# Optimization experiments

Hardware: AMD Instinct MI355X
Metric: run time of the kernel (lower is better)

The kernel has to match this reference:

```python
import jax, jax.numpy as jnp
import numpy as np

BS = 4
EMBED = 256
HEADS = 8
LEVELS = 4
POINTS = 4
HD = EMBED // HEADS  # 32
SHAPES = np.array([[96, 96], [48, 48], [24, 24], [12, 12]], dtype=np.int64)
LQ = int((SHAPES[:, 0] * SHAPES[:, 1]).sum())  # 12240


def _offset_bias():
    # faithful to MSDeformableAttention._reset_parameters grid init
    thetas = np.arange(HEADS, dtype=np.float32) * (2.0 * np.pi / HEADS)
    g = np.stack([np.cos(thetas), np.sin(thetas)], -1)
    g = g / np.abs(g).max(-1, keepdims=True)
    g = np.tile(g.reshape(HEADS, 1, 1, 2), (1, LEVELS, POINTS, 1))
    g = g * np.arange(1, POINTS + 1, dtype=np.float32).reshape(1, 1, -1, 1)
    return jnp.asarray(g.reshape(-1), dtype=jnp.float32)


def setup_inputs() -> dict:
    key = jax.random.key(0)
    ks = jax.random.split(key, 8)
    tp = HEADS * LEVELS * POINTS
    d = {}
    d["query"] = jax.random.normal(ks[0], (BS, LQ, EMBED), jnp.float32)
    d["reference_points"] = jax.random.uniform(ks[1], (BS, LQ, LEVELS, 2), jnp.float32)
    d["value"] = jax.random.normal(ks[2], (BS, LQ, EMBED), jnp.float32)
    d["value_spatial_shapes"] = SHAPES  # static numpy, int
    d["W_off"] = jax.random.normal(ks[3], (EMBED, tp * 2), jnp.float32) * 0.01
    d["b_off"] = _offset_bias()
    d["W_attn"] = jax.random.normal(ks[4], (EMBED, tp), jnp.float32) * 0.02
    d["b_attn"] = jnp.zeros((tp,), jnp.float32)
    d["W_val"] = jax.random.normal(ks[5], (EMBED, EMBED), jnp.float32) * (1.0 / np.sqrt(EMBED).astype(np.float32))
    d["b_val"] = jnp.zeros((EMBED,), jnp.float32)
    d["W_out"] = jax.random.normal(ks[6], (EMBED, EMBED), jnp.float32) * (1.0 / np.sqrt(EMBED).astype(np.float32))
    d["b_out"] = jnp.zeros((EMBED,), jnp.float32)
    return d


def _bilinear_sample(img, grid):
    # img: [B,H,W,C]; grid: [B,Q,P,2] in [-1,1] (x,y)
    # matches F.grid_sample(mode='bilinear', padding_mode='zeros', align_corners=False)
    B, H, W, C = img.shape
    gx = (grid[..., 0] + 1.0) * (W * 0.5) - 0.5
    gy = (grid[..., 1] + 1.0) * (H * 0.5) - 0.5
    x0 = jnp.floor(gx)
    y0 = jnp.floor(gy)
    wx = gx - x0
    wy = gy - y0
    x0i = x0.astype(jnp.int32)
    y0i = y0.astype(jnp.int32)
    x1i = x0i + 1
    y1i = y0i + 1
    flat = img.reshape(B, H * W, C)

    def corner(xi, yi, w):
        valid = (xi >= 0) & (xi < W) & (yi >= 0) & (yi < H)
        idx = jnp.clip(yi, 0, H - 1) * W + jnp.clip(xi, 0, W - 1)
        v = jnp.take_along_axis(flat, idx.reshape(B, -1, 1), axis=1)
        v = v.reshape(idx.shape + (C,))
        return v * (w * valid)[..., None]

    return (corner(x0i, y0i, (1.0 - wx) * (1.0 - wy))
            + corner(x1i, y0i, wx * (1.0 - wy))
            + corner(x0i, y1i, (1.0 - wx) * wy)
            + corner(x1i, y1i, wx * wy))


def reference(query, reference_points, value, value_spatial_shapes,
              W_off, b_off, W_attn, b_attn, W_val, b_val, W_out, b_out):
    shapes = np.asarray(value_spatial_shapes)  # static [L,2] (H,W)
    bs, Lq, _ = query.shape
    v = (value @ W_val + b_val).reshape(bs, -1, HEADS, HD)  # [bs,Lv,H,hd]
    off = (query @ W_off + b_off).reshape(bs, Lq, HEADS, LEVELS, POINTS, 2)
    aw = jax.nn.softmax((query @ W_attn + b_attn).reshape(bs, Lq, HEADS, LEVELS * POINTS), axis=-1)
    aw = aw.reshape(bs, Lq, HEADS, LEVELS, POINTS)
    # normalizer is (W,H) per level
    norm = jnp.asarray(shapes[:, ::-1].copy(), jnp.float32).reshape(1, 1, 1, LEVELS, 1, 2)
    loc = reference_points[:, :, None, :, None, :] + off / norm
    grids = 2.0 * loc - 1.0  # [bs,Lq,H,L,P,2]

    acc = jnp.zeros((bs * HEADS, Lq, HD), query.dtype)
    start = 0
    for lvl in range(LEVELS):
        h, w = int(shapes[lvl, 0]), int(shapes[lvl, 1])
        v_l = v[:, start:start + h * w].reshape(bs, h, w, HEADS, HD)
        v_l = v_l.transpose(0, 3, 1, 2, 4).reshape(bs * HEADS, h, w, HD)
        g_l = grids[:, :, :, lvl].transpose(0, 2, 1, 3, 4).reshape(bs * HEADS, Lq, POINTS, 2)
        s_l = _bilinear_sample(v_l, g_l)  # [bs*H, Lq, P, hd]
        w_l = aw[:, :, :, lvl].transpose(0, 2, 1, 3).reshape(bs * HEADS, Lq, POINTS)
        acc = acc + jnp.einsum('bqpc,bqp->bqc', s_l, w_l)
        start += h * w

    out = acc.reshape(bs, HEADS, Lq, HD).transpose(0, 2, 1, 3).reshape(bs, Lq, EMBED)
    return out @ W_out + b_out
```

## Files before the change

### kernel.cpp

```cpp
#include <hip/hip_runtime.h>
#include <hip/hip_bf16.h>

static constexpr int BS     = 4;
static constexpr int EMBED  = 256;
static constexpr int HEADS  = 8;
static constexpr int LEVELS = 4;
static constexpr int POINTS = 4;
static constexpr int HD     = 32;
static constexpr int LQ     = 12240;
static constexpr int NROW   = BS * LQ;
static constexpr int LVL_W[4]  = {96, 48, 24, 12};
static constexpr int LVL_H[4]  = {96, 48, 24, 12};
static constexpr int LVL_ST[4] = {0, 9216, 11520, 12096};

typedef __attribute__((ext_vector_type(8))) short short8;
typedef __attribute__((ext_vector_type(4))) float f32x4;
typedef __attribute__((ext_vector_type(2))) float f32x2;

__device__ __forceinline__ unsigned short f2bf(float f) {
    unsigned int u = __float_as_uint(f);
    unsigned int r = (u + 0x7FFFu + ((u >> 16) & 1u)) >> 16;
    return (unsigned short)r;
}

__device__ __forceinline__ void pkfma(f32x2& a, f32x2 v, f32x2 w) {
    asm("v_pk_fma_f32 %0, %1, %2, %0" : "+v"(a) : "v"(v), "v"(w));
}

__global__ __launch_bounds__(256) void prep_weights(
    const float* __restrict__ W_off, const float* __restrict__ W_attn,
    const float* __restrict__ W_val, const float* __restrict__ W_out,
    unsigned short* __restrict__ WT_oa, unsigned short* __restrict__ WT_val,
    unsigned short* __restrict__ WT_out)
{
    const int gid = blockIdx.x * 256 + threadIdx.x;
    const int k = gid & 255;
    const int n = gid >> 8;
    if (n < 384) {
        const float v = (n < 256) ? W_off[k * 256 + n] : W_attn[k * 128 + (n - 256)];
        WT_oa[n * 256 + k] = f2bf(v);
    } else if (n < 640) {
        const int nn = n - 384;
        WT_val[nn * 256 + k] = f2bf(W_val[k * 256 + nn]);
    } else {
        const int nn = n - 640;
        WT_out[nn * 256 + k] = f2bf(W_out[k * 256 + nn]);
    }
}

__global__ __launch_bounds__(256, 5) void gemm_vo(
    const float* __restrict__ Aval, const float* __restrict__ Aqry,
    const unsigned short* __restrict__ Wval, const unsigned short* __restrict__ Woa,
    const float* __restrict__ bval, const float* __restrict__ boff,
    const float* __restrict__ battn,
    unsigned short* __restrict__ Vout, float* __restrict__ OAout)
{
    constexpr int NTW = 2;
    constexpr int NB  = 128;
    constexpr int K   = 256;
    __shared__ __align__(16) unsigned short As[64][40];
    __shared__ __align__(16) unsigned short Bs[NB][40];

    const int x    = blockIdx.x;
    const bool isV = (x < 2);
    const float* A = isV ? Aval : Aqry;
    const unsigned short* Wt = isV ? Wval : Woa;
    const int n0   = isV ? x * 128 : (x - 2) * 128;

    const int tid = threadIdx.x;
    const int m0 = blockIdx.y * 64;
    const int w  = tid >> 6;
    const int l  = tid & 63;
    const int lm = l & 15;
    const int lq = l >> 4;

    const int sr = tid >> 2;
    const int kg = (tid & 3) * 8;

    float4 pa0, pa1;
    short8 pb[NTW];

    auto gload = [&](int k0) {
        const float* ap = &A[(size_t)(m0 + sr) * K + k0 + kg];
        pa0 = *(const float4*)ap;
        pa1 = *(const float4*)(ap + 4);
        #pragma unroll
        for (int i = 0; i < NTW; ++i) {
            const int slot = tid + i * 256;
            const int n  = slot >> 2;
            const int kk = (slot & 3) * 8;
            pb[i] = *(const short8*)&Wt[(size_t)(n0 + n) * K + k0 + kk];
        }
    };

    f32x4 acc[4][NTW];
    #pragma unroll
    for (int rg = 0; rg < 4; ++rg)
        #pragma unroll
        for (int nt = 0; nt < NTW; ++nt)
            acc[rg][nt] = (f32x4){0.f, 0.f, 0.f, 0.f};

    gload(0);
    #pragma unroll 2
    for (int k0 = 0; k0 < K; k0 += 32) {
        uint4 pk;
        pk.x = (unsigned int)f2bf(pa0.x) | ((unsigned int)f2bf(pa0.y) << 16);
        pk.y = (unsigned int)f2bf(pa0.z) | ((unsigned int)f2bf(pa0.w) << 16);
        pk.z = (unsigned int)f2bf(pa1.x) | ((unsigned int)f2bf(pa1.y) << 16);
        pk.w = (unsigned int)f2bf(pa1.z) | ((unsigned int)f2bf(pa1.w) << 16);
        *(uint4*)&As[sr][kg] = pk;
        #pragma unroll
        for (int i = 0; i < NTW; ++i) {
            const int slot = tid + i * 256;
            const int n  = slot >> 2;
            const int kk = (slot & 3) * 8;
            *(short8*)&Bs[n][kk] = pb[i];
        }
        __syncthreads();

        if (k0 + 32 < K) gload(k0 + 32);

        short8 af[4];
        #pragma unroll
        for (int rg = 0; rg < 4; ++rg)
            af[rg] = *(const short8*)&As[rg * 16 + lm][lq * 8];
        #pragma unroll
        for (int nt = 0; nt < NTW; ++nt) {
            const short8 bf = *(const short8*)&Bs[(w * NTW + nt) * 16 + lm][lq * 8];
            #pragma unroll
            for (int rg = 0; rg < 4; ++rg)
                acc[rg][nt] = __builtin_amdgcn_mfma_f32_16x16x32_bf16(af[rg], bf, acc[rg][nt], 0, 0, 0);
        }
        __syncthreads();
    }

    #pragma unroll
    for (int nt = 0; nt < NTW; ++nt) {
        const int col = n0 + (w * NTW + nt) * 16 + lm;
        float b;
        if (isV) b = bval[col];
        else     b = (col < 256) ? boff[col] : battn[col - 256];
        #pragma unroll
        for (int rg = 0; rg < 4; ++rg)
            #pragma unroll
            for (int r = 0; r < 4; ++r) {
                const int row = m0 + rg * 16 + lq * 4 + r;
                const float v = acc[rg][nt][r] + b;
                if (isV) Vout[(size_t)row * 256 + col] = f2bf(v);
                else     OAout[(size_t)row * 384 + col] = v;
            }
    }
}

template <int NTW, bool A_BF16, bool OUT_BF16>
__global__ __launch_bounds__(256, 5) void gemm_mfma(
    const void* __restrict__ Av, const unsigned short* __restrict__ Wt,
    const float* __restrict__ bias0, const float* __restrict__ bias1, int nsplit,
    void* __restrict__ Cv, int N)
{
    constexpr int NB = NTW * 64;
    constexpr int K  = 256;
    __shared__ __align__(16) unsigned short As[64][40];
    __shared__ __align__(16) unsigned short Bs[NB][40];

    const int tid = threadIdx.x;
    const int m0 = blockIdx.y * 64;
    const int n0 = blockIdx.x * NB;
    const int w  = tid >> 6;
    const int l  = tid & 63;
    const int lm = l & 15;
    const int lq = l >> 4;

    const int sr = tid >> 2;
    const int kg = (tid & 3) * 8;

    float4 pa0, pa1; short8 pa_bf;
    short8 pb[NTW];

    auto gload = [&](int k0) {
        if (A_BF16) {
            const unsigned short* A = (const unsigned short*)Av;
            pa_bf = *(const short8*)&A[(size_t)(m0 + sr) * K + k0 + kg];
        } else {
            const float* A = (const float*)Av;
            const float* ap = &A[(size_t)(m0 + sr) * K + k0 + kg];
            pa0 = *(const float4*)ap;
            pa1 = *(const float4*)(ap + 4);
        }
        #pragma unroll
        for (int i = 0; i < NTW; ++i) {
            const int slot = tid + i * 256;
            const int n  = slot >> 2;
            const int kk = (slot & 3) * 8;
            pb[i] = *(const short8*)&Wt[(size_t)(n0 + n) * K + k0 + kk];
        }
    };

    f32x4 acc[4][NTW];
    #pragma unroll
    for (int rg = 0; rg < 4; ++rg)
        #pragma unroll
        for (int nt = 0; nt < NTW; ++nt)
            acc[rg][nt] = (f32x4){0.f, 0.f, 0.f, 0.f};

    gload(0);
    #pragma unroll 2
    for (int k0 = 0; k0 < K; k0 += 32) {
        if (A_BF16) {
            *(short8*)&As[sr][kg] = pa_bf;
        } else {
            uint4 pk;
            pk.x = (unsigned int)f2bf(pa0.x) | ((unsigned int)f2bf(pa0.y) << 16);
            pk.y = (unsigned int)f2bf(pa0.z) | ((unsigned int)f2bf(pa0.w) << 16);
            pk.z = (unsigned int)f2bf(pa1.x) | ((unsigned int)f2bf(pa1.y) << 16);
            pk.w = (unsigned int)f2bf(pa1.z) | ((unsigned int)f2bf(pa1.w) << 16);
            *(uint4*)&As[sr][kg] = pk;
        }
        #pragma unroll
        for (int i = 0; i < NTW; ++i) {
            const int slot = tid + i * 256;
            const int n  = slot >> 2;
            const int kk = (slot & 3) * 8;
            *(short8*)&Bs[n][kk] = pb[i];
        }
        __syncthreads();

        if (k0 + 32 < K) gload(k0 + 32);

        short8 af[4];
        #pragma unroll
        for (int rg = 0; rg < 4; ++rg)
            af[rg] = *(const short8*)&As[rg * 16 + lm][lq * 8];
        #pragma unroll
        for (int nt = 0; nt < NTW; ++nt) {
            const short8 bf = *(const short8*)&Bs[(w * NTW + nt) * 16 + lm][lq * 8];
            #pragma unroll
            for (int rg = 0; rg < 4; ++rg)
                acc[rg][nt] = __builtin_amdgcn_mfma_f32_16x16x32_bf16(af[rg], bf, acc[rg][nt], 0, 0, 0);
        }
        __syncthreads();
    }

    #pragma unroll
    for (int nt = 0; nt < NTW; ++nt) {
        const int col = n0 + (w * NTW + nt) * 16 + lm;
        const float b = (col < nsplit) ? bias0[col] : bias1[col - nsplit];
        #pragma unroll
        for (int rg = 0; rg < 4; ++rg)
            #pragma unroll
            for (int r = 0; r < 4; ++r) {
                const int row = m0 + rg * 16 + lq * 4 + r;
                const float v = acc[rg][nt][r] + b;
                if (OUT_BF16) ((unsigned short*)Cv)[(size_t)row * N + col] = f2bf(v);
                else          ((float*)Cv)[(size_t)row * N + col] = v;
            }
    }
}

__global__ __launch_bounds__(256, 6) void sample_kernel(
    const unsigned short* __restrict__ V,
    const float* __restrict__ OA,
    const float* __restrict__ refp,
    unsigned short* __restrict__ ACC)
{
    __shared__ __align__(16) unsigned int pr_o[512][4];
    __shared__ __align__(16) unsigned int pr_w[512][4];

    const int tid = threadIdx.x;

    const unsigned bx = blockIdx.x;
    const int xcd  = bx & 7;
    const int slot = bx >> 3;
    const int batch = xcd >> 1;
    const int wb   = slot * 2 + (xcd & 1);
    const int row0 = batch * LQ + wb * 4;

    {
        float4* dst = (float4*)pr_o;
        const float4* src = (const float4*)(OA + (size_t)row0 * 384);
        dst[tid] = src[tid];
        if (tid < 128) dst[tid + 256] = src[tid + 256];
        __syncthreads();

        const int g = tid & 31;
        const int r = g >> 3;
        const int h = g & 7;
        const int L = tid >> 5;
        const float* rowp = (const float*)pr_o + r * 384;

        const float lg0 = rowp[256 + h * 16 + L];
        const float lg1 = rowp[256 + h * 16 + L + 8];

        float* smax = (float*)pr_w;
        float* ssum = smax + 264;
        smax[L * 33 + g] = fmaxf(lg0, lg1);
        __syncthreads();
        float m = smax[g];
        #pragma unroll
        for (int k = 1; k < 8; ++k) m = fmaxf(m, smax[k * 33 + g]);
        const float e0 = __expf(lg0 - m);
        const float e1 = __expf(lg1 - m);
        ssum[L * 33 + g] = e0 + e1;
        __syncthreads();
        float sden = ssum[g];
        #pragma unroll
        for (int k = 1; k < 8; ++k) sden += ssum[k * 33 + g];
        const float inv = 1.0f / sden;

        uint4 ostash[2], wstash[2];
        int   sidx[2];
        #pragma unroll
        for (int ss = 0; ss < 2; ++ss) {
            const int lp  = L + ss * 8;
            const int s   = lp * 32 + g;
            const int lvl = lp >> 2;
            const int Wl = LVL_W[lvl], Hl = LVL_H[lvl], st = LVL_ST[lvl];

            const float2 oxy = *(const float2*)&rowp[h * 32 + lp * 2];
            const float2 rxy = *(const float2*)&refp[(size_t)(row0 + r) * 8 + lvl * 2];
            const float wgt = (ss ? e1 : e0) * inv;

            const float gx = (rxy.x + oxy.x / (float)Wl) * (float)Wl - 0.5f;
            const float gy = (rxy.y + oxy.y / (float)Hl) * (float)Hl - 0.5f;

            const float fx = floorf(gx), fy = floorf(gy);
            const float wx = gx - fx,    wy = gy - fy;
            const int x0 = (int)fx, y0 = (int)fy;
            const int x1 = x0 + 1,  y1 = y0 + 1;

            const bool bx0 = ((unsigned)x0 < (unsigned)Wl);
            const bool bx1 = ((unsigned)x1 < (unsigned)Wl);
            const bool by0 = ((unsigned)y0 < (unsigned)Hl);
            const bool by1 = ((unsigned)y1 < (unsigned)Hl);
            const float w00 = (bx0 && by0) ? (1.f - wx) * (1.f - wy) * wgt : 0.f;
            const float w10 = (bx1 && by0) ? wx * (1.f - wy) * wgt : 0.f;
            const float w01 = (bx0 && by1) ? (1.f - wx) * wy * wgt : 0.f;
            const float w11 = (bx1 && by1) ? wx * wy * wgt : 0.f;

            const int cx0 = min(max(x0, 0), Wl - 1);
            const int cx1 = min(max(x1, 0), Wl - 1);
            const int cy0 = min(max(y0, 0), Hl - 1);
            const int cy1 = min(max(y1, 0), Hl - 1);

            uint4 o;
            o.x = (unsigned int)(st + cy0 * Wl + cx0) * 512u;
            o.y = (unsigned int)(st + cy0 * Wl + cx1) * 512u;
            o.z = (unsigned int)(st + cy1 * Wl + cx0) * 512u;
            o.w = (unsigned int)(st + cy1 * Wl + cx1) * 512u;
            ostash[ss] = o;

            uint4 wv;
            wv.x = __float_as_uint(w00); wv.y = __float_as_uint(w10);
            wv.z = __float_as_uint(w01); wv.w = __float_as_uint(w11);
            wstash[ss] = wv;
            sidx[ss] = s;
        }
        __syncthreads();
        *(uint4*)&pr_o[sidx[0]][0] = ostash[0];
        *(uint4*)&pr_o[sidx[1]][0] = ostash[1];
        *(uint4*)&pr_w[sidx[0]][0] = wstash[0];
        *(uint4*)&pr_w[sidx[1]][0] = wstash[1];
    }
    __syncthreads();

    const int w    = tid >> 6;
    const int l    = tid & 63;
    const int half = l >> 5;
    const int head = (l >> 2) & 7;
    const int c16  = (l & 3) * 16;

    const int row  = __builtin_amdgcn_readfirstlane(row0 + w);
    const char* vrow = (const char*)V + (size_t)batch * ((size_t)LQ * 512);
    const unsigned int lane_byte = (unsigned int)(head * 64 + c16);
    const int sid0 = half * 256 + w * 8 + head;

    uint4 ofs[2];
    f32x4 wv[2];
    uint4 dat[2][4];
    f32x2 accA[4], accB[4];
    #pragma unroll
    for (int i = 0; i < 4; ++i) { accA[i] = (f32x2){0.f,0.f}; accB[i] = (f32x2){0.f,0.f}; }

    auto ldglb = [&](int buf) {
        const uint4 o = ofs[buf];
        dat[buf][0] = *(const uint4*)(vrow + (lane_byte + o.x));
        dat[buf][1] = *(const uint4*)(vrow + (lane_byte + o.y));
        dat[buf][2] = *(const uint4*)(vrow + (lane_byte + o.z));
        dat[buf][3] = *(const uint4*)(vrow + (lane_byte + o.w));
    };
    auto ldpr = [&](int j, int buf) {
        ofs[buf] = *(const uint4*)&pr_o[sid0 + j * 32][0];
        wv[buf]  = *(const f32x4*)&pr_w[sid0 + j * 32][0];
    };
    auto pkstep = [&](f32x2& A, f32x2& B, unsigned u0, unsigned u1, f32x2 w2) {
        f32x2 pa, pb;
        pa.x = __uint_as_float(u0 << 16);
        pa.y = __uint_as_float(u1 << 16);
        pb.x = __uint_as_float(u0 & 0xffff0000u);
        pb.y = __uint_as_float(u1 & 0xffff0000u);
        pkfma(A, pa, w2);
        pkfma(B, pb, w2);
    };
    auto consume = [&](int buf) {
        f32x2 w01; w01.x = wv[buf].x; w01.y = wv[buf].y;
        f32x2 w23; w23.x = wv[buf].z; w23.y = wv[buf].w;
        const uint4 d0 = dat[buf][0], d1 = dat[buf][1];
        pkstep(accA[0], accB[0], d0.x, d1.x, w01);
        pkstep(accA[1], accB[1], d0.y, d1.y, w01);
        pkstep(accA[2], accB[2], d0.z, d1.z, w01);
        pkstep(accA[3], accB[3], d0.w, d1.w, w01);
        const uint4 d2 = dat[buf][2], d3 = dat[buf][3];
        pkstep(accA[0], accB[0], d2.x, d3.x, w23);
        pkstep(accA[1], accB[1], d2.y, d3.y, w23);
        pkstep(accA[2], accB[2], d2.z, d3.z, w23);
        pkstep(accA[3], accB[3], d2.w, d3.w, w23);
    };

    ldpr(0, 0);
    ldpr(1, 1);
    ldglb(0);
    #pragma unroll
    for (int j = 0; j < 8; ++j) {
        if (j + 1 < 8) ldglb((j + 1) & 1);
        consume(j & 1);
        if (j + 2 < 8) ldpr(j + 2, j & 1);
    }

    float c[8];
    #pragma unroll
    for (int i = 0; i < 4; ++i) {
        c[2 * i]     = accA[i].x + accA[i].y;
        c[2 * i + 1] = accB[i].x + accB[i].y;
    }
    #pragma unroll
    for (int i = 0; i < 8; ++i) c[i] += __shfl_xor(c[i], 32);

    if (half == 0) {
        uint4 o;
        o.x = (unsigned int)f2bf(c[0]) | ((unsigned int)f2bf(c[1]) << 16);
        o.y = (unsigned int)f2bf(c[2]) | ((unsigned int)f2bf(c[3]) << 16);
        o.z = (unsigned int)f2bf(c[4]) | ((unsigned int)f2bf(c[5]) << 16);
        o.w = (unsigned int)f2bf(c[6]) | ((unsigned int)f2bf(c[7]) << 16);
        *(uint4*)((char*)(ACC + (size_t)row * EMBED) + head * 64 + c16) = o;
    }
}

extern "C" void kernel_launch(void* const* d_in, const int* in_sizes, int n_in,
                              void* d_out, int out_size, void* d_ws, size_t ws_size,
                              hipStream_t stream) {
    const float* query  = (const float*)d_in[0];
    const float* refp   = (const float*)d_in[1];
    const float* value  = (const float*)d_in[2];
    const float* W_off  = (const float*)d_in[4];
    const float* b_off  = (const float*)d_in[5];
    const float* W_attn = (const float*)d_in[6];
    const float* b_attn = (const float*)d_in[7];
    const float* W_val  = (const float*)d_in[8];
    const float* b_val  = (const float*)d_in[9];
    const float* W_out  = (const float*)d_in[10];
    const float* b_out  = (const float*)d_in[11];
    float* out = (float*)d_out;

    unsigned short* WT_oa  = (unsigned short*)d_ws;
    unsigned short* WT_val = WT_oa  + 384 * 256;
    unsigned short* WT_out = WT_val + 256 * 256;
    unsigned short* V      = WT_out + 256 * 256;
    float*          OA     = (float*)(V + (size_t)NROW * EMBED);
    unsigned short* ACCb   = (unsigned short*)(OA + (size_t)NROW * 384);

    dim3 blk(256);

    prep_weights<<<896, blk, 0, stream>>>(W_off, W_attn, W_val, W_out,
                                          WT_oa, WT_val, WT_out);
    gemm_vo<<<dim3(5, NROW / 64), blk, 0, stream>>>(
        value, query, WT_val, WT_oa, b_val, b_off, b_attn, V, OA);
    sample_kernel<<<NROW / 4, blk, 0, stream>>>(V, OA, refp, ACCb);
    gemm_mfma<2, true, false><<<dim3(2, NROW / 64), blk, 0, stream>>>(
        ACCb, WT_out, b_out, b_out, 256, out, 256);
}
```

Measured before the change: 332.3 us.

## Store value projection as fp16 and use dot2 for bilinear accumulation

The value projection is now written as fp16 instead of bf16, and the bilinear weights are packed as fp16 pairs. The sampling inner loop then uses v_dot2_f32_f16 on byte-permuted value pairs in place of bf16 unpacking plus packed FMA, which cuts the ALU work per sample. The sample kernel also drops the LDS staging of the offset/attention rows and reads them straight from global memory. A smaller weight buffer lets it raise occupancy to 7 waves. The trade is fp16 range and precision risk for values and weights, and uncoalesced global reads in the prologue.

```diff
diff --git a/kernel.cpp b/kernel.cpp
--- a/kernel.cpp
+++ b/kernel.cpp
@@ -16,6 +16,7 @@
 typedef __attribute__((ext_vector_type(8))) short short8;
 typedef __attribute__((ext_vector_type(4))) float f32x4;
 typedef __attribute__((ext_vector_type(2))) float f32x2;
+typedef _Float16 h2 __attribute__((ext_vector_type(2)));
 
 __device__ __forceinline__ unsigned short f2bf(float f) {
     unsigned int u = __float_as_uint(f);
@@ -23,8 +24,20 @@
     return (unsigned short)r;
 }
 
-__device__ __forceinline__ void pkfma(f32x2& a, f32x2 v, f32x2 w) {
-    asm("v_pk_fma_f32 %0, %1, %2, %0" : "+v"(a) : "v"(v), "v"(w));
+__device__ __forceinline__ unsigned int pkh(float a, float b) {
+    const unsigned int ua = __builtin_bit_cast(unsigned short, (_Float16)a);
+    const unsigned int ub = __builtin_bit_cast(unsigned short, (_Float16)b);
+    return ua | (ub << 16);
+}
+
+__device__ __forceinline__ float dot2(float acc, unsigned int v, unsigned int w) {
+#if __has_builtin(__builtin_amdgcn_fdot2)
+    return __builtin_amdgcn_fdot2(__builtin_bit_cast(h2, v),
+                                  __builtin_bit_cast(h2, w), acc, false);
+#else
+    asm("v_dot2_f32_f16 %0, %1, %2, %0" : "+v"(acc) : "v"(v), "v"(w));
+    return acc;
+#endif
 }
 
 __global__ __launch_bounds__(256) void prep_weights(
@@ -146,7 +159,8 @@
             for (int r = 0; r < 4; ++r) {
                 const int row = m0 + rg * 16 + lq * 4 + r;
                 const float v = acc[rg][nt][r] + b;
-                if (isV) Vout[(size_t)row * 256 + col] = f2bf(v);
+                if (isV) Vout[(size_t)row * 256 + col] =
+                             __builtin_bit_cast(unsigned short, (_Float16)v);
                 else     OAout[(size_t)row * 384 + col] = v;
             }
     }
@@ -257,14 +271,14 @@
     }
 }
 
-__global__ __launch_bounds__(256, 6) void sample_kernel(
+__global__ __launch_bounds__(256, 7) void sample_kernel(
     const unsigned short* __restrict__ V,
     const float* __restrict__ OA,
     const float* __restrict__ refp,
     unsigned short* __restrict__ ACC)
 {
     __shared__ __align__(16) unsigned int pr_o[512][4];
-    __shared__ __align__(16) unsigned int pr_w[512][4];
+    __shared__ __align__(16) unsigned int pr_w[512][2];
 
     const int tid = threadIdx.x;
 
@@ -276,17 +290,12 @@
     const int row0 = batch * LQ + wb * 4;
 
     {
-        float4* dst = (float4*)pr_o;
-        const float4* src = (const float4*)(OA + (size_t)row0 * 384);
-        dst[tid] = src[tid];
-        if (tid < 128) dst[tid + 256] = src[tid + 256];
-        __syncthreads();
-
         const int g = tid & 31;
         const int r = g >> 3;
         const int h = g & 7;
         const int L = tid >> 5;
-        const float* rowp = (const float*)pr_o + r * 384;
+        const int prow = row0 + r;
+        const float* rowp = OA + (size_t)prow * 384;
 
         const float lg0 = rowp[256 + h * 16 + L];
         const float lg1 = rowp[256 + h * 16 + L + 8];
@@ -307,7 +316,7 @@
         for (int k = 1; k < 8; ++k) sden += ssum[k * 33 + g];
         const float inv = 1.0f / sden;
 
-        uint4 ostash[2], wstash[2];
+        uint2 wstash[2];
         int   sidx[2];
         #pragma unroll
         for (int ss = 0; ss < 2; ++ss) {
@@ -317,7 +326,7 @@
             const int Wl = LVL_W[lvl], Hl = LVL_H[lvl], st = LVL_ST[lvl];
 
             const float2 oxy = *(const float2*)&rowp[h * 32 + lp * 2];
-            const float2 rxy = *(const float2*)&refp[(size_t)(row0 + r) * 8 + lvl * 2];
+            const float2 rxy = *(const float2*)&refp[(size_t)prow * 8 + lvl * 2];
             const float wgt = (ss ? e1 : e0) * inv;
 
             const float gx = (rxy.x + oxy.x / (float)Wl) * (float)Wl - 0.5f;
@@ -347,19 +356,14 @@
             o.y = (unsigned int)(st + cy0 * Wl + cx1) * 512u;
             o.z = (unsigned int)(st + cy1 * Wl + cx0) * 512u;
             o.w = (unsigned int)(st + cy1 * Wl + cx1) * 512u;
-            ostash[ss] = o;
-
-            uint4 wv;
-            wv.x = __float_as_uint(w00); wv.y = __float_as_uint(w10);
-            wv.z = __float_as_uint(w01); wv.w = __float_as_uint(w11);
-            wstash[ss] = wv;
+            *(uint4*)&pr_o[s][0] = o;
+
+            wstash[ss] = make_uint2(pkh(w00, w10), pkh(w01, w11));
             sidx[ss] = s;
         }
         __syncthreads();
-        *(uint4*)&pr_o[sidx[0]][0] = ostash[0];
-        *(uint4*)&pr_o[sidx[1]][0] = ostash[1];
-        *(uint4*)&pr_w[sidx[0]][0] = wstash[0];
-        *(uint4*)&pr_w[sidx[1]][0] = wstash[1];
+        *(uint2*)&pr_w[sidx[0]][0] = wstash[0];
+        *(uint2*)&pr_w[sidx[1]][0] = wstash[1];
     }
     __syncthreads();
 
@@ -374,12 +378,15 @@
     const unsigned int lane_byte = (unsigned int)(head * 64 + c16);
     const int sid0 = half * 256 + w * 8 + head;
 
+    constexpr unsigned SEL_LO = 0x01000504u;
+    constexpr unsigned SEL_HI = 0x03020706u;
+
     uint4 ofs[2];
-    f32x4 wv[2];
+    uint2 wpk[2];
     uint4 dat[2][4];
-    f32x2 accA[4], accB[4];
-    #pragma unroll
-    for (int i = 0; i < 4; ++i) { accA[i] = (f32x2){0.f,0.f}; accB[i] = (f32x2){0.f,0.f}; }
+    float acc[8];
+    #pragma unroll
+    for (int i = 0; i < 8; ++i) acc[i] = 0.f;
 
     auto ldglb = [&](int buf) {
         const uint4 o = ofs[buf];
@@ -390,30 +397,21 @@
     };
     auto ldpr = [&](int j, int buf) {
         ofs[buf] = *(const uint4*)&pr_o[sid0 + j * 32][0];
-        wv[buf]  = *(const f32x4*)&pr_w[sid0 + j * 32][0];
-    };
-    auto pkstep = [&](f32x2& A, f32x2& B, unsigned u0, unsigned u1, f32x2 w2) {
-        f32x2 pa, pb;
-        pa.x = __uint_as_float(u0 << 16);
-        pa.y = __uint_as_float(u1 << 16);
-        pb.x = __uint_as_float(u0 & 0xffff0000u);
-        pb.y = __uint_as_float(u1 & 0xffff0000u);
-        pkfma(A, pa, w2);
-        pkfma(B, pb, w2);
+        wpk[buf] = *(const uint2*)&pr_w[sid0 + j * 32][0];
+    };
+    auto cpair = [&](const uint4& d0, const uint4& d1, unsigned wp) {
+        acc[0] = dot2(acc[0], __builtin_amdgcn_perm(d0.x, d1.x, SEL_LO), wp);
+        acc[1] = dot2(acc[1], __builtin_amdgcn_perm(d0.x, d1.x, SEL_HI), wp);
+        acc[2] = dot2(acc[2], __builtin_amdgcn_perm(d0.y, d1.y, SEL_LO), wp);
+        acc[3] = dot2(acc[3], __builtin_amdgcn_perm(d0.y, d1.y, SEL_HI), wp);
+        acc[4] = dot2(acc[4], __builtin_amdgcn_perm(d0.z, d1.z, SEL_LO), wp);
+        acc[5] = dot2(acc[5], __builtin_amdgcn_perm(d0.z, d1.z, SEL_HI), wp);
+        acc[6] = dot2(acc[6], __builtin_amdgcn_perm(d0.w, d1.w, SEL_LO), wp);
+        acc[7] = dot2(acc[7], __builtin_amdgcn_perm(d0.w, d1.w, SEL_HI), wp);
     };
     auto consume = [&](int buf) {
-        f32x2 w01; w01.x = wv[buf].x; w01.y = wv[buf].y;
-        f32x2 w23; w23.x = wv[buf].z; w23.y = wv[buf].w;
-        const uint4 d0 = dat[buf][0], d1 = dat[buf][1];
-        pkstep(accA[0], accB[0], d0.x, d1.x, w01);
-        pkstep(accA[1], accB[1], d0.y, d1.y, w01);
-        pkstep(accA[2], accB[2], d0.z, d1.z, w01);
-        pkstep(accA[3], accB[3], d0.w, d1.w, w01);
-        const uint4 d2 = dat[buf][2], d3 = dat[buf][3];
-        pkstep(accA[0], accB[0], d2.x, d3.x, w23);
-        pkstep(accA[1], accB[1], d2.y, d3.y, w23);
-        pkstep(accA[2], accB[2], d2.z, d3.z, w23);
-        pkstep(accA[3], accB[3], d2.w, d3.w, w23);
+        cpair(dat[buf][0], dat[buf][1], wpk[buf].x);
+        cpair(dat[buf][2], dat[buf][3], wpk[buf].y);
     };
 
     ldpr(0, 0);
@@ -426,21 +424,15 @@
         if (j + 2 < 8) ldpr(j + 2, j & 1);
     }
 
-    float c[8];
-    #pragma unroll
-    for (int i = 0; i < 4; ++i) {
-        c[2 * i]     = accA[i].x + accA[i].y;
-        c[2 * i + 1] = accB[i].x + accB[i].y;
-    }
-    #pragma unroll
-    for (int i = 0; i < 8; ++i) c[i] += __shfl_xor(c[i], 32);
+    #pragma unroll
+    for (int i = 0; i < 8; ++i) acc[i] += __shfl_xor(acc[i], 32);
 
     if (half == 0) {
         uint4 o;
-        o.x = (unsigned int)f2bf(c[0]) | ((unsigned int)f2bf(c[1]) << 16);
-        o.y = (unsigned int)f2bf(c[2]) | ((unsigned int)f2bf(c[3]) << 16);
-        o.z = (unsigned int)f2bf(c[4]) | ((unsigned int)f2bf(c[5]) << 16);
-        o.w = (unsigned int)f2bf(c[6]) | ((unsigned int)f2bf(c[7]) << 16);
+        o.x = (unsigned int)f2bf(acc[0]) | ((unsigned int)f2bf(acc[1]) << 16);
+        o.y = (unsigned int)f2bf(acc[2]) | ((unsigned int)f2bf(acc[3]) << 16);
+        o.z = (unsigned int)f2bf(acc[4]) | ((unsigned int)f2bf(acc[5]) << 16);
+        o.w = (unsigned int)f2bf(acc[6]) | ((unsigned int)f2bf(acc[7]) << 16);
         *(uint4*)((char*)(ACC + (size_t)row * EMBED) + head * 64 + c16) = o;
     }
 }
```

Measured after the change: 341.0 us. 2.6% more time.
